# Kernel optimization log

Measured on AMD Instinct MI355X. Metric: run time of the kernel, lower is better.

Reference implementation:

```python
import jax, jax.numpy as jnp
import numpy as np

EMBED_DIM = 1024
NUM_HEADS = 16
HEAD_DIM = EMBED_DIM // NUM_HEADS
SCALING = HEAD_DIM ** -0.5


def setup_inputs() -> dict:
    key = jax.random.key(0)
    ks = jax.random.split(key, 10)
    T, B, E = 2048, 2, EMBED_DIM
    s = 0.02
    return {
        "query": jax.random.normal(ks[0], (T, B, E), jnp.float32),
        "key_padding_mask": jnp.zeros((B, T), jnp.bool_),
        "attn_mask": jnp.zeros((T, T), jnp.float32),
        "Wq": jax.random.normal(ks[1], (E, E), jnp.float32) * s,
        "bq": jnp.zeros((E,), jnp.float32),
        "Wk": jax.random.normal(ks[2], (E, E), jnp.float32) * s,
        "bk": jnp.zeros((E,), jnp.float32),
        "Wv": jax.random.normal(ks[3], (E, E), jnp.float32) * s,
        "bv": jnp.zeros((E,), jnp.float32),
        "Wo": jax.random.normal(ks[4], (E, E), jnp.float32) * s,
        "bo": jnp.zeros((E,), jnp.float32),
    }


def reference(query, key_padding_mask, attn_mask, Wq, bq, Wk, bk, Wv, bv, Wo, bo):
    T, B, E = query.shape
    H, D = NUM_HEADS, HEAD_DIM
    # projections (nn.Linear: x @ W.T + b)
    q = (query @ Wq.T + bq) * SCALING
    k_new = query @ Wk.T + bk  # returned as new_keys
    v_new = query @ Wv.T + bv  # returned as new_values
    S = T  # self-attention, no cache
    # [T, B, E] -> [B*H, T, D]
    qh = q.reshape(T, B * H, D).transpose(1, 0, 2)
    kh = k_new.reshape(S, B * H, D).transpose(1, 0, 2)
    vh = v_new.reshape(S, B * H, D).transpose(1, 0, 2)
    # scores: [B*H, T, S]
    scores = jnp.einsum("btd,bsd->bts", qh, kh)
    scores = scores + attn_mask[None, :, :]
    # key padding mask: [B, S] -> broadcast over heads / tgt
    scores = scores.reshape(B, H, T, S)
    scores = jnp.where(key_padding_mask[:, None, None, :], -jnp.inf, scores)
    scores = scores.reshape(B * H, T, S)
    attn_weights = jax.nn.softmax(scores.astype(jnp.float32), axis=-1)
    attn_probs = attn_weights.astype(query.dtype)  # dropout p=0.0
    out = jnp.einsum("bts,bsd->btd", attn_probs, vh)  # [B*H, T, D]
    out = out.transpose(1, 0, 2).reshape(T, B, E)
    attn_output = out @ Wo.T + bo
    return (attn_output, attn_weights.reshape(B, H, T, S), k_new, v_new)
```

## Files before the change

kernel.cpp:

```cpp
#include <hip/hip_runtime.h>
#include <hip/hip_bf16.h>
#include <stdint.h>

typedef __bf16 bf16_t;
typedef __bf16 bf16x8 __attribute__((ext_vector_type(8)));
typedef float f32x4 __attribute__((ext_vector_type(4)));

#define SCALING 0.125f
#define EXPBIAS 20.0f

#define WS_XQ  (0u)
#define WS_W   (8u << 20)
#define WS_QH  (16u << 20)
#define WS_KH  (24u << 20)
#define WS_VT  (32u << 20)
#define WS_X2  (40u << 20)
#define WS_AM  (48u << 20)

#define OFF_OUT 0
#define OFF_WEI 4194304
#define OFF_K   138412032
#define OFF_V   142606336

typedef const __attribute__((address_space(1))) void gvoid_t;
typedef __attribute__((address_space(3))) void lvoid_t;

__device__ inline void gload_lds16(const void* g, void* l) {
  __builtin_amdgcn_global_load_lds((gvoid_t*)g, (lvoid_t*)l, 16, 0, 0);
}

__global__ __launch_bounds__(256) void cvt_kernel(const float* __restrict__ s,
                                                  bf16_t* __restrict__ d, int n4) {
  int i = blockIdx.x * 256 + threadIdx.x;
  if (i < n4) {
    float4 v = ((const float4*)s)[i];
    union { bf16_t h[4]; uint2 u; } o;
    o.h[0] = (bf16_t)v.x; o.h[1] = (bf16_t)v.y;
    o.h[2] = (bf16_t)v.z; o.h[3] = (bf16_t)v.w;
    ((uint2*)d)[i] = o.u;
  }
}

__global__ __launch_bounds__(256) void cvtw_kernel(const float* __restrict__ w0,
                                                   const float* __restrict__ w1,
                                                   const float* __restrict__ w2,
                                                   const float* __restrict__ w3,
                                                   bf16_t* __restrict__ dst) {
  const float* src = blockIdx.y == 0 ? w0 : blockIdx.y == 1 ? w1 : blockIdx.y == 2 ? w2 : w3;
  bf16_t* d = dst + (size_t)blockIdx.y * 1048576;
  int i = blockIdx.x * 256 + threadIdx.x;
  float4 v = ((const float4*)src)[i];
  union { bf16_t h[4]; uint2 u; } o;
  o.h[0] = (bf16_t)v.x; o.h[1] = (bf16_t)v.y;
  o.h[2] = (bf16_t)v.z; o.h[3] = (bf16_t)v.w;
  ((uint2*)d)[i] = o.u;
}

__global__ __launch_bounds__(256) void amask_prep(const float* __restrict__ am,
                                                  float* __restrict__ af) {
  int o = blockIdx.x * 256 + threadIdx.x;
  if (o >= (1 << 20)) return;
  int lane = o & 63;
  int f = o >> 6;
  int st = f & 15;
  int wslab = (f >> 4) & 7;
  int tt = f >> 7;
  int t = tt * 16 + (lane & 15);
  int s = wslab * 256 + 32 * (st >> 1) + 4 * (st & 1) + 8 * (lane >> 4);
  float4 v = *(const float4*)&am[(size_t)t * 2048 + s];
  v.x -= EXPBIAS; v.y -= EXPBIAS; v.z -= EXPBIAS; v.w -= EXPBIAS;
  *(float4*)&af[(size_t)o * 4] = v;
}

__global__ __launch_bounds__(256) void gemm_nt(
    const bf16_t* __restrict__ Xq, const bf16_t* __restrict__ X2,
    const bf16_t* __restrict__ Wall,
    const float* __restrict__ bq, const float* __restrict__ bk,
    const float* __restrict__ bv, const float* __restrict__ bo,
    float* __restrict__ dout,
    bf16_t* __restrict__ qh, bf16_t* __restrict__ kh, bf16_t* __restrict__ vT,
    int mode_base) {
  const int mode = mode_base + blockIdx.z;
  const bf16_t* __restrict__ X = (mode < 3) ? Xq : X2;
  const bf16_t* __restrict__ W = Wall + (size_t)mode * 1048576;
  const float* __restrict__ bias = (mode == 0) ? bq : (mode == 1) ? bk : (mode == 2) ? bv : bo;

  __shared__ alignas(16) bf16_t Alds[128 * 64];
  __shared__ alignas(16) bf16_t Blds[128 * 64];

  const int lane = threadIdx.x & 63;
  const int w = threadIdx.x >> 6;
  const int wr = w >> 1, wc = w & 1;
  const int m0 = blockIdx.y * 128, n0 = blockIdx.x * 128;

  f32x4 acc[4][4] = {};

  for (int kk = 0; kk < 1024; kk += 64) {
    __syncthreads();
    const int rb = w * 32;
#pragma unroll
    for (int i = 0; i < 4; ++i) {
      int r = rb + i * 8 + (lane >> 3);
      int c = (lane & 7) * 8;
      gload_lds16(X + (size_t)(m0 + r) * 1024 + kk + c, &Alds[(rb + i * 8) * 64]);
      gload_lds16(W + (size_t)(n0 + r) * 1024 + kk + c, &Blds[(rb + i * 8) * 64]);
    }
    __syncthreads();
#pragma unroll
    for (int kx = 0; kx < 2; ++kx) {
      bf16x8 af[4], bfr[4];
#pragma unroll
      for (int mi = 0; mi < 4; ++mi)
        af[mi] = *(const bf16x8*)&Alds[(wr * 64 + mi * 16 + (lane & 15)) * 64 + kx * 32 + (lane >> 4) * 8];
#pragma unroll
      for (int ni = 0; ni < 4; ++ni)
        bfr[ni] = *(const bf16x8*)&Blds[(wc * 64 + ni * 16 + (lane & 15)) * 64 + kx * 32 + (lane >> 4) * 8];
#pragma unroll
      for (int mi = 0; mi < 4; ++mi)
#pragma unroll
        for (int ni = 0; ni < 4; ++ni)
          acc[mi][ni] = __builtin_amdgcn_mfma_f32_16x16x32_bf16(af[mi], bfr[ni], acc[mi][ni], 0, 0, 0);
    }
  }

#pragma unroll
  for (int mi = 0; mi < 4; ++mi) {
#pragma unroll
    for (int ni = 0; ni < 4; ++ni) {
#pragma unroll
      for (int r = 0; r < 4; ++r) {
        int i = m0 + wr * 64 + mi * 16 + (lane >> 4) * 4 + r;
        int j = n0 + wc * 64 + ni * 16 + (lane & 15);
        float v = acc[mi][ni][r] + bias[j];
        int t = i >> 1, b = i & 1, h = j >> 6, d = j & 63;
        int bh = b * 16 + h;
        if (mode == 0) {
          qh[(size_t)bh * 131072 + t * 64 + d] = (bf16_t)(v * SCALING);
        } else if (mode == 1) {
          dout[OFF_K + (size_t)i * 1024 + j] = v;
          int s = t;
          int idx = ((((s >> 5) * 2 + ((s >> 2) & 1)) * 2 + (d >> 5)) * 64 +
                     ((d >> 3) & 3) * 16 + 4 * ((s >> 3) & 3) + (s & 3)) * 8 + (d & 7);
          kh[(size_t)bh * 131072 + idx] = (bf16_t)v;
        } else if (mode == 2) {
          dout[OFF_V + (size_t)i * 1024 + j] = v;
          int s = t;
          int idx = (((s >> 5) * 4 + (d >> 4)) * 64 +
                     ((s >> 3) & 3) * 16 + (d & 15)) * 8 + (s & 7);
          vT[(size_t)bh * 131072 + idx] = (bf16_t)v;
        } else {
          dout[OFF_OUT + (size_t)i * 1024 + j] = v;
        }
      }
    }
  }
}

#define ALOAD(n, K0, K1, MV, KU)                                                   \
  {                                                                                \
    const int fi_ = (w * 8 + ((n) >> 1)) * 4 + ((n) & 1) * 2;                      \
    K0 = *(const bf16x8*)&kfrag[(size_t)fi_ * 512 + lane * 8];                     \
    K1 = *(const bf16x8*)&kfrag[(size_t)(fi_ + 1) * 512 + lane * 8];               \
    MV = *(const float4*)&afrag[(n) * 256 + lane * 4];                             \
    KU = *(const uint32_t*)&kpm[b * 2048 + s0w + 32 * ((n) >> 1) + 4 * ((n) & 1) + 8 * g]; \
  }

__global__ __launch_bounds__(512, 4) void attn_kernel(
    const bf16_t* __restrict__ qh, const bf16_t* __restrict__ kh,
    const bf16_t* __restrict__ vT,
    const float* __restrict__ amaskF, const uint8_t* __restrict__ kpm,
    float* __restrict__ wout, bf16_t* __restrict__ X2) {
  const int lane = threadIdx.x & 63;
  const int w = threadIdx.x >> 6;
  const int lt = lane & 15;
  const int g = lane >> 4;
  const int bh = blockIdx.x;
  const int tt = blockIdx.y;
  const int t0 = tt * 16;
  const int b = bh >> 4;

  __shared__ float wsum[16][8];
  __shared__ float pbuf[8][16][68];
  __shared__ float sbuf[8][16][33];

  const bf16_t* __restrict__ qbase = qh + (size_t)bh * 131072;
  const bf16_t* __restrict__ kfrag = kh + (size_t)bh * 131072;
  const bf16_t* __restrict__ vfrag = vT + (size_t)bh * 131072;
  const float* __restrict__ afrag = amaskF + ((size_t)(tt * 8 + w) * 16) * 256;
  float* __restrict__ wrow = wout + (size_t)bh * 4194304;
  const int s0w = w * 256;

  bf16x8 aq[2];
#pragma unroll
  for (int kx = 0; kx < 2; ++kx)
    aq[kx] = *(const bf16x8*)&qbase[(t0 + lt) * 64 + kx * 32 + g * 8];

  bf16x8 pa[8];
  float ssum = 0.f;

  bf16x8 ka0, ka1, kb0, kb1, kc0, kc1;
  float4 ma, mb, mc;
  uint32_t ua, ub, uc;
  ALOAD(0, ka0, ka1, ma, ua);
  ALOAD(1, kb0, kb1, mb, ub);
#pragma unroll
  for (int st = 0; st < 16; ++st) {
    if (st < 14) {
      ALOAD(st + 2, kc0, kc1, mc, uc);
    }
    f32x4 acc = {0.f, 0.f, 0.f, 0.f};
    acc = __builtin_amdgcn_mfma_f32_16x16x32_bf16(ka0, aq[0], acc, 0, 0, 0);
    acc = __builtin_amdgcn_mfma_f32_16x16x32_bf16(ka1, aq[1], acc, 0, 0, 0);
#pragma unroll
    for (int r = 0; r < 4; ++r) {
      float m = (r == 0) ? ma.x : (r == 1) ? ma.y : (r == 2) ? ma.z : ma.w;
      float val = acc[r] + m;
      val = ((ua >> (8 * r)) & 0xff) ? -__builtin_inff() : val;
      float e = __expf(val);
      ssum += e;
      pa[st >> 1][4 * (st & 1) + r] = (bf16_t)e;
    }
    ka0 = kb0; ka1 = kb1; ma = mb; ua = ub;
    kb0 = kc0; kb1 = kc1; mb = mc; ub = uc;
  }

  ssum += __shfl_xor(ssum, 16, 64);
  ssum += __shfl_xor(ssum, 32, 64);
  if (lane < 16) wsum[lane][w] = ssum;
  __syncthreads();
  float ss = 0.f;
#pragma unroll
  for (int ww = 0; ww < 8; ++ww) ss += wsum[lt][ww];
  const float rl = 1.0f / ss;

  f32x4 po[4] = {};
  bf16x8 vfa[4], vfb[4];
#pragma unroll
  for (int dt = 0; dt < 4; ++dt)
    vfa[dt] = *(const bf16x8*)&vfrag[(size_t)((w * 8) * 4 + dt) * 512 + lane * 8];
#pragma unroll
  for (int kx = 0; kx < 8; ++kx) {
    if (kx < 7) {
#pragma unroll
      for (int dt = 0; dt < 4; ++dt)
        vfb[dt] = *(const bf16x8*)&vfrag[(size_t)((w * 8 + kx + 1) * 4 + dt) * 512 + lane * 8];
    }
    f32x4 wv0, wv1;
#pragma unroll
    for (int r = 0; r < 4; ++r) { wv0[r] = (float)pa[kx][r] * rl; wv1[r] = (float)pa[kx][4 + r] * rl; }
    *(f32x4*)&sbuf[w][lt][8 * g] = wv0;
    *(f32x4*)&sbuf[w][lt][8 * g + 4] = wv1;
    __builtin_amdgcn_s_setprio(1);
#pragma unroll
    for (int dt = 0; dt < 4; ++dt)
      po[dt] = __builtin_amdgcn_mfma_f32_16x16x32_bf16(vfa[dt], pa[kx], po[dt], 0, 0, 0);
    __builtin_amdgcn_s_setprio(0);
    asm volatile("s_waitcnt lgkmcnt(0)" ::: "memory");
#pragma unroll
    for (int p = 0; p < 2; ++p) {
      int row = 8 * p + (lane >> 3);
      int c4 = (lane & 7) * 4;
      f32x4 rv = *(const f32x4*)&sbuf[w][row][c4];
      __builtin_nontemporal_store(rv,
          (f32x4*)&wrow[(size_t)(t0 + row) * 2048 + s0w + 32 * kx + c4]);
    }
#pragma unroll
    for (int dt = 0; dt < 4; ++dt) vfa[dt] = vfb[dt];
  }
#pragma unroll
  for (int dt = 0; dt < 4; ++dt) po[dt] *= rl;

#pragma unroll
  for (int dt = 0; dt < 4; ++dt) {
    f32x4 v = po[dt];
    *(f32x4*)&pbuf[w][lt][dt * 16 + 4 * g] = v;
  }
  __syncthreads();
  int e0 = threadIdx.x * 2;
  int row = e0 >> 6, d = e0 & 63;
  float v0 = 0.f, v1 = 0.f;
#pragma unroll
  for (int ww = 0; ww < 8; ++ww) {
    v0 += pbuf[ww][row][d];
    v1 += pbuf[ww][row][d + 1];
  }
  int h = bh & 15;
  union { bf16_t hh[2]; uint32_t u; } pk;
  pk.hh[0] = (bf16_t)v0; pk.hh[1] = (bf16_t)v1;
  *(uint32_t*)&X2[(size_t)((t0 + row) * 2 + b) * 1024 + h * 64 + d] = pk.u;
}

extern "C" void kernel_launch(void* const* d_in, const int* in_sizes, int n_in,
                              void* d_out, int out_size, void* d_ws, size_t ws_size,
                              hipStream_t stream) {
  (void)in_sizes; (void)n_in; (void)out_size; (void)ws_size;
  const float* query = (const float*)d_in[0];
  const uint8_t* kpm = (const uint8_t*)d_in[1];
  const float* amask = (const float*)d_in[2];
  const float* Wq = (const float*)d_in[3];
  const float* bq = (const float*)d_in[4];
  const float* Wk = (const float*)d_in[5];
  const float* bk = (const float*)d_in[6];
  const float* Wv = (const float*)d_in[7];
  const float* bv = (const float*)d_in[8];
  const float* Wo = (const float*)d_in[9];
  const float* bo = (const float*)d_in[10];
  float* dout = (float*)d_out;
  char* ws = (char*)d_ws;

  bf16_t* Xq = (bf16_t*)(ws + WS_XQ);
  bf16_t* Wbf = (bf16_t*)(ws + WS_W);
  bf16_t* qh = (bf16_t*)(ws + WS_QH);
  bf16_t* kh = (bf16_t*)(ws + WS_KH);
  bf16_t* vT = (bf16_t*)(ws + WS_VT);
  bf16_t* X2 = (bf16_t*)(ws + WS_X2);
  float* amF = (float*)(ws + WS_AM);

  cvt_kernel<<<4096, 256, 0, stream>>>(query, Xq, 1048576);
  cvtw_kernel<<<dim3(1024, 4), 256, 0, stream>>>(Wq, Wk, Wv, Wo, Wbf);
  amask_prep<<<4096, 256, 0, stream>>>(amask, amF);
  gemm_nt<<<dim3(8, 32, 3), 256, 0, stream>>>(Xq, X2, Wbf, bq, bk, bv, bo, dout, qh, kh, vT, 0);
  attn_kernel<<<dim3(32, 128), 512, 0, stream>>>(qh, kh, vT, amF, kpm, dout + OFF_WEI, X2);
  gemm_nt<<<dim3(8, 32, 1), 256, 0, stream>>>(Xq, X2, Wbf, bq, bk, bv, bo, dout, qh, kh, vT, 3);
}
```

Measured before the change: 263.8 us.

## Stage K/V epilogue through LDS for coalesced fragment stores; merge prep kernels

```diff
diff --git a/kernel.cpp b/kernel.cpp
--- a/kernel.cpp
+++ b/kernel.cpp
@@ -29,49 +29,47 @@
   __builtin_amdgcn_global_load_lds((gvoid_t*)g, (lvoid_t*)l, 16, 0, 0);
 }
 
-__global__ __launch_bounds__(256) void cvt_kernel(const float* __restrict__ s,
-                                                  bf16_t* __restrict__ d, int n4) {
-  int i = blockIdx.x * 256 + threadIdx.x;
-  if (i < n4) {
-    float4 v = ((const float4*)s)[i];
+__global__ __launch_bounds__(256) void prep_kernel(
+    const float* __restrict__ q,
+    const float* __restrict__ w0, const float* __restrict__ w1,
+    const float* __restrict__ w2, const float* __restrict__ w3,
+    const float* __restrict__ am,
+    bf16_t* __restrict__ Xq, bf16_t* __restrict__ Wbf, float* __restrict__ af) {
+  const int blk = blockIdx.x;
+  const int tid = threadIdx.x;
+  if (blk < 4096) {
+    int i = blk * 256 + tid;
+    float4 v = ((const float4*)q)[i];
     union { bf16_t h[4]; uint2 u; } o;
     o.h[0] = (bf16_t)v.x; o.h[1] = (bf16_t)v.y;
     o.h[2] = (bf16_t)v.z; o.h[3] = (bf16_t)v.w;
-    ((uint2*)d)[i] = o.u;
-  }
-}
-
-__global__ __launch_bounds__(256) void cvtw_kernel(const float* __restrict__ w0,
-                                                   const float* __restrict__ w1,
-                                                   const float* __restrict__ w2,
-                                                   const float* __restrict__ w3,
-                                                   bf16_t* __restrict__ dst) {
-  const float* src = blockIdx.y == 0 ? w0 : blockIdx.y == 1 ? w1 : blockIdx.y == 2 ? w2 : w3;
-  bf16_t* d = dst + (size_t)blockIdx.y * 1048576;
-  int i = blockIdx.x * 256 + threadIdx.x;
-  float4 v = ((const float4*)src)[i];
-  union { bf16_t h[4]; uint2 u; } o;
-  o.h[0] = (bf16_t)v.x; o.h[1] = (bf16_t)v.y;
-  o.h[2] = (bf16_t)v.z; o.h[3] = (bf16_t)v.w;
-  ((uint2*)d)[i] = o.u;
-}
-
-__global__ __launch_bounds__(256) void amask_prep(const float* __restrict__ am,
-                                                  float* __restrict__ af) {
-  int o = blockIdx.x * 256 + threadIdx.x;
-  if (o >= (1 << 20)) return;
-  int lane = o & 63;
-  int f = o >> 6;
-  int st = f & 15;
-  int wslab = (f >> 4) & 7;
-  int tt = f >> 7;
-  int t = tt * 16 + (lane & 15);
-  int s = wslab * 256 + 32 * (st >> 1) + 4 * (st & 1) + 8 * (lane >> 4);
-  float4 v = *(const float4*)&am[(size_t)t * 2048 + s];
-  v.x -= EXPBIAS; v.y -= EXPBIAS; v.z -= EXPBIAS; v.w -= EXPBIAS;
-  *(float4*)&af[(size_t)o * 4] = v;
-}
-
+    ((uint2*)Xq)[i] = o.u;
+  } else if (blk < 8192) {
+    int i = (blk - 4096) * 256 + tid;
+    int wsel = i >> 18;
+    int loc = i & 262143;
+    const float* src = (wsel == 0) ? w0 : (wsel == 1) ? w1 : (wsel == 2) ? w2 : w3;
+    float4 v = ((const float4*)src)[loc];
+    union { bf16_t h[4]; uint2 u; } o;
+    o.h[0] = (bf16_t)v.x; o.h[1] = (bf16_t)v.y;
+    o.h[2] = (bf16_t)v.z; o.h[3] = (bf16_t)v.w;
+    ((uint2*)(Wbf + (size_t)wsel * 1048576))[loc] = o.u;
+  } else {
+    int o = (blk - 8192) * 256 + tid;
+    int lane = o & 63;
+    int f = o >> 6;
+    int st = f & 15;
+    int wslab = (f >> 4) & 7;
+    int tt = f >> 7;
+    int t = tt * 16 + (lane & 15);
+    int s = wslab * 256 + 32 * (st >> 1) + 4 * (st & 1) + 8 * (lane >> 4);
+    float4 v = *(const float4*)&am[(size_t)t * 2048 + s];
+    v.x -= EXPBIAS; v.y -= EXPBIAS; v.z -= EXPBIAS; v.w -= EXPBIAS;
+    *(float4*)&af[(size_t)o * 4] = v;
+  }
+}
+
+#define CSTRIDE 134
 __global__ __launch_bounds__(256) void gemm_nt(
     const bf16_t* __restrict__ Xq, const bf16_t* __restrict__ X2,
     const bf16_t* __restrict__ Wall,
@@ -85,8 +83,9 @@
   const bf16_t* __restrict__ W = Wall + (size_t)mode * 1048576;
   const float* __restrict__ bias = (mode == 0) ? bq : (mode == 1) ? bk : (mode == 2) ? bv : bo;
 
-  __shared__ alignas(16) bf16_t Alds[128 * 64];
-  __shared__ alignas(16) bf16_t Blds[128 * 64];
+  __shared__ alignas(16) bf16_t SM[128 * CSTRIDE];
+  bf16_t* Alds = SM;
+  bf16_t* Blds = SM + 8192;
 
   const int lane = threadIdx.x & 63;
   const int w = threadIdx.x >> 6;
@@ -123,33 +122,69 @@
     }
   }
 
-#pragma unroll
-  for (int mi = 0; mi < 4; ++mi) {
-#pragma unroll
-    for (int ni = 0; ni < 4; ++ni) {
-#pragma unroll
-      for (int r = 0; r < 4; ++r) {
-        int i = m0 + wr * 64 + mi * 16 + (lane >> 4) * 4 + r;
-        int j = n0 + wc * 64 + ni * 16 + (lane & 15);
-        float v = acc[mi][ni][r] + bias[j];
-        int t = i >> 1, b = i & 1, h = j >> 6, d = j & 63;
-        int bh = b * 16 + h;
-        if (mode == 0) {
-          qh[(size_t)bh * 131072 + t * 64 + d] = (bf16_t)(v * SCALING);
-        } else if (mode == 1) {
-          dout[OFF_K + (size_t)i * 1024 + j] = v;
-          int s = t;
-          int idx = ((((s >> 5) * 2 + ((s >> 2) & 1)) * 2 + (d >> 5)) * 64 +
-                     ((d >> 3) & 3) * 16 + 4 * ((s >> 3) & 3) + (s & 3)) * 8 + (d & 7);
-          kh[(size_t)bh * 131072 + idx] = (bf16_t)v;
-        } else if (mode == 2) {
-          dout[OFF_V + (size_t)i * 1024 + j] = v;
-          int s = t;
-          int idx = (((s >> 5) * 4 + (d >> 4)) * 64 +
-                     ((s >> 3) & 3) * 16 + (d & 15)) * 8 + (s & 7);
-          vT[(size_t)bh * 131072 + idx] = (bf16_t)v;
-        } else {
-          dout[OFF_OUT + (size_t)i * 1024 + j] = v;
+  if (mode == 1 || mode == 2) {
+    __syncthreads();
+#pragma unroll
+    for (int mi = 0; mi < 4; ++mi) {
+#pragma unroll
+      for (int ni = 0; ni < 4; ++ni) {
+#pragma unroll
+        for (int r = 0; r < 4; ++r) {
+          int il = wr * 64 + mi * 16 + (lane >> 4) * 4 + r;
+          int jl = wc * 64 + ni * 16 + (lane & 15);
+          float v = acc[mi][ni][r] + bias[n0 + jl];
+          dout[(mode == 1 ? OFF_K : OFF_V) + (size_t)(m0 + il) * 1024 + n0 + jl] = v;
+          SM[il * CSTRIDE + jl] = (bf16_t)v;
+        }
+      }
+    }
+    __syncthreads();
+    const int s0 = m0 >> 1;
+    const int b_ = w >> 1;
+    const int hl = w & 1;
+    const int bh = b_ * 16 + (n0 >> 6) + hl;
+    if (mode == 1) {
+      bf16_t* dst = kh + (size_t)bh * 131072;
+#pragma unroll
+      for (int f = 0; f < 8; ++f) {
+        int sbl = f >> 2, par = (f >> 1) & 1, dh = f & 1;
+        int il = 2 * (sbl * 32 + ((lane >> 2) & 3) * 8 + par * 4 + (lane & 3)) + b_;
+        int jl = hl * 64 + dh * 32 + (lane >> 4) * 8;
+        bf16x8 fr = *(const bf16x8*)&SM[il * CSTRIDE + jl];
+        int fi = ((s0 >> 5) + sbl) * 4 + par * 2 + dh;
+        *(bf16x8*)&dst[(size_t)fi * 512 + lane * 8] = fr;
+      }
+    } else {
+      bf16_t* dst = vT + (size_t)bh * 131072;
+#pragma unroll
+      for (int f = 0; f < 8; ++f) {
+        int sbl = f >> 2, dq = f & 3;
+        int jl = hl * 64 + dq * 16 + (lane & 15);
+        int il0 = 2 * (sbl * 32 + (lane >> 4) * 8) + b_;
+        bf16x8 fr;
+#pragma unroll
+        for (int e = 0; e < 8; ++e) fr[e] = SM[(il0 + 2 * e) * CSTRIDE + jl];
+        int fi = ((s0 >> 5) + sbl) * 4 + dq;
+        *(bf16x8*)&dst[(size_t)fi * 512 + lane * 8] = fr;
+      }
+    }
+  } else {
+#pragma unroll
+    for (int mi = 0; mi < 4; ++mi) {
+#pragma unroll
+      for (int ni = 0; ni < 4; ++ni) {
+#pragma unroll
+        for (int r = 0; r < 4; ++r) {
+          int i = m0 + wr * 64 + mi * 16 + (lane >> 4) * 4 + r;
+          int j = n0 + wc * 64 + ni * 16 + (lane & 15);
+          float v = acc[mi][ni][r] + bias[j];
+          int t = i >> 1, b = i & 1, h = j >> 6, d = j & 63;
+          int bh = b * 16 + h;
+          if (mode == 0) {
+            qh[(size_t)bh * 131072 + t * 64 + d] = (bf16_t)(v * SCALING);
+          } else {
+            dout[OFF_OUT + (size_t)i * 1024 + j] = v;
+          }
         }
       }
     }
@@ -316,9 +351,7 @@
   bf16_t* X2 = (bf16_t*)(ws + WS_X2);
   float* amF = (float*)(ws + WS_AM);
 
-  cvt_kernel<<<4096, 256, 0, stream>>>(query, Xq, 1048576);
-  cvtw_kernel<<<dim3(1024, 4), 256, 0, stream>>>(Wq, Wk, Wv, Wo, Wbf);
-  amask_prep<<<4096, 256, 0, stream>>>(amask, amF);
+  prep_kernel<<<12288, 256, 0, stream>>>(query, Wq, Wk, Wv, Wo, amask, Xq, Wbf, amF);
   gemm_nt<<<dim3(8, 32, 3), 256, 0, stream>>>(Xq, X2, Wbf, bq, bk, bv, bo, dout, qh, kh, vT, 0);
   attn_kernel<<<dim3(32, 128), 512, 0, stream>>>(qh, kh, vT, amF, kpm, dout + OFF_WEI, X2);
   gemm_nt<<<dim3(8, 32, 1), 256, 0, stream>>>(Xq, X2, Wbf, bq, bk, bv, bo, dout, qh, kh, vT, 3);
```

New measurement: 249.5 us. -5.4%, faster.
